# Kernel tuning notes

Hardware: AMD Instinct MI355X
Metric: run time of the kernel (lower is better)

## Reference

```python
import jax, jax.numpy as jnp
import numpy as np

B, T, D_IN, D_MODEL = 4, 4096, 256, 128


def setup_inputs() -> dict:
    key = jax.random.key(0)
    ks = jax.random.split(key, 7)
    s_in = 1.0 / np.sqrt(D_IN)
    return {
        "x": jax.random.normal(ks[0], (B, T, D_IN), dtype=jnp.float32),
        "Wq": jax.random.normal(ks[1], (D_IN, D_MODEL), dtype=jnp.float32) * s_in,
        "bq": jnp.zeros((D_MODEL,), dtype=jnp.float32),
        "Wk": jax.random.normal(ks[2], (D_IN, D_MODEL), dtype=jnp.float32) * s_in,
        "bk": jnp.zeros((D_MODEL,), dtype=jnp.float32),
        "Wv": jax.random.normal(ks[3], (D_IN, D_MODEL), dtype=jnp.float32) * s_in,
        "bv": jnp.zeros((D_MODEL,), dtype=jnp.float32),
    }


def reference(x, Wq, bq, Wk, bk, Wv, bv):
    # projections: (B,T,d_in) @ (d_in,d_model) -> (B,T,d_model)
    q = x @ Wq + bq
    k = x @ Wk + bk
    v = x @ Wv + bv
    # scores: (B,T,T), scaled by sqrt(d_model)
    scores = jnp.einsum("btd,bsd->bts", q, k) / np.sqrt(D_MODEL).astype(np.float32)
    attn = jax.nn.softmax(scores, axis=-1)
    out = jnp.einsum("bts,bsd->btd", attn, v)
    return out, attn
```

## Files before the change

### kernel.cpp

```cpp
#include <hip/hip_runtime.h>
#include <hip/hip_bf16.h>
#include <stdint.h>

#define TT 4096
#define DM 128
#define DIN 256
#define NB 4

typedef __attribute__((ext_vector_type(4))) float f32x4;
typedef __attribute__((ext_vector_type(8))) short s16x8;
typedef __attribute__((ext_vector_type(4))) short s16x4;

__device__ __forceinline__ unsigned short f2bf(float f) {
    union { float f; unsigned int u; } v; v.f = f;
    return (unsigned short)((v.u + 0x7FFFu + ((v.u >> 16) & 1u)) >> 16);
}
__device__ __forceinline__ float bf2f(unsigned short h) {
    union { unsigned int u; float f; } v; v.u = ((unsigned int)h) << 16;
    return v.f;
}

__device__ __forceinline__ void cp16(const void* g, void* l) {
    __builtin_amdgcn_global_load_lds(
        (__attribute__((address_space(1))) unsigned int*)(size_t)g,
        (__attribute__((address_space(3))) unsigned int*)l, 16, 0, 0);
}

__global__ __launch_bounds__(256) void k_wt(const float* __restrict__ Wq,
                                            const float* __restrict__ Wk,
                                            const float* __restrict__ Wv,
                                            unsigned short* __restrict__ Wtb) {
    int tid = blockIdx.x * 256 + threadIdx.x;
    int m = tid >> 15;
    int r = tid & 32767;
    int n = r >> 8;
    int k = r & 255;
    const float* W = (m == 0) ? Wq : (m == 1) ? Wk : Wv;
    Wtb[(size_t)tid] = f2bf(W[k * DM + n]);
}

__global__ __launch_bounds__(256) void k_proj(const float* __restrict__ x,
        const float* __restrict__ bq, const float* __restrict__ bk, const float* __restrict__ bv,
        const unsigned short* __restrict__ Wtb,
        unsigned short* __restrict__ Qb, unsigned short* __restrict__ Kb,
        unsigned short* __restrict__ Vb) {
    __shared__ __align__(16) unsigned short wt[DM][40];
    __shared__ __align__(16) unsigned short xl[64][40];
    int m = blockIdx.x >> 8;
    int tile = blockIdx.x & 255;
    int rowbase = tile * 64;
    int i = threadIdx.x;
    int w = i >> 6, l = i & 63;
    int lg = l >> 4, ll = l & 15;
    const float* bias = (m == 0) ? bq : (m == 1) ? bk : bv;
    unsigned short* out = (m == 0) ? Qb : (m == 1) ? Kb : Vb;
    const unsigned short* wsrc = Wtb + (size_t)m * DM * DIN;

    f32x4 acc[8];
    for (int n = 0; n < 8; n++) acc[n] = (f32x4){0.f, 0.f, 0.f, 0.f};

    for (int kk = 0; kk < 8; kk++) {
        int k0 = kk * 32;
        for (int t = 0; t < 2; t++) {
            int idx = i + t * 256;
            int row = idx >> 2, c8 = idx & 3;
            s16x8 v = *(const s16x8*)(wsrc + (size_t)row * DIN + k0 + c8 * 8);
            *(s16x8*)(&wt[row][c8 * 8]) = v;
        }
        for (int t = 0; t < 2; t++) {
            int idx = i + t * 256;
            int row = idx >> 3, c4 = idx & 7;
            f32x4 v = *(const f32x4*)(x + (size_t)(rowbase + row) * DIN + k0 + c4 * 4);
            s16x4 h;
            for (int j = 0; j < 4; j++) h[j] = (short)f2bf(v[j]);
            *(s16x4*)(&xl[row][c4 * 4]) = h;
        }
        __syncthreads();
        s16x8 a = *(const s16x8*)(&xl[w * 16 + ll][lg * 8]);
        for (int n = 0; n < 8; n++) {
            s16x8 b = *(const s16x8*)(&wt[n * 16 + ll][lg * 8]);
            acc[n] = __builtin_amdgcn_mfma_f32_16x16x32_bf16(a, b, acc[n], 0, 0, 0);
        }
        __syncthreads();
    }
    for (int n = 0; n < 8; n++) {
        int col = n * 16 + ll;
        float bv_ = bias[col];
        for (int j = 0; j < 4; j++) {
            int row = rowbase + w * 16 + lg * 4 + j;
            out[(size_t)row * DM + col] = f2bf(acc[n][j] + bv_);
        }
    }
}

__global__ __launch_bounds__(256) void k_vt(const unsigned short* __restrict__ Vb,
                                            unsigned short* __restrict__ Vtb) {
    __shared__ __align__(16) unsigned short tile[64][72];
    int bid = blockIdx.x;
    int b = bid >> 7;
    int rem = bid & 127;
    int tI = rem >> 1, dI = rem & 1;
    int t0 = tI * 64, d0 = dI * 64;
    int i = threadIdx.x;
    for (int t = 0; t < 2; t++) {
        int idx = i + t * 256;
        int r = idx >> 3, c8 = idx & 7;
        s16x8 v = *(const s16x8*)(Vb + ((size_t)(b * TT) + t0 + r) * DM + d0 + c8 * 8);
        *(s16x8*)(&tile[r][c8 * 8]) = v;
    }
    __syncthreads();
    for (int t = 0; t < 2; t++) {
        int idx = i + t * 256;
        int r2 = idx >> 3, c8 = idx & 7;
        s16x8 v;
        for (int j = 0; j < 8; j++) v[j] = (short)tile[c8 * 8 + j][r2];
        *(s16x8*)(Vtb + ((size_t)b * DM + d0 + r2) * TT + t0 + c8 * 8) = v;
    }
}

__global__ __launch_bounds__(256, 4) void k_rowsum(const unsigned short* __restrict__ Qb,
        const unsigned short* __restrict__ Kb, float* __restrict__ rsum8) {
    __shared__ __align__(16) char smem[24576];

    int bid = blockIdx.x;
    int id2 = (bid & 7) * 256 + (bid >> 3);
    int b = id2 >> 9;
    int rem = id2 & 511;
    int rt = rem >> 2, kq = rem & 3;
    int rowbase = rt * 32;
    int i = threadIdx.x;
    int w = i >> 6, l = i & 63;
    int rg = w & 1, ks = w >> 1;
    int lg = l >> 4, ll = l & 15;

    const unsigned short* Qrow = Qb + ((size_t)(b * TT) + rowbase) * DM;
    const unsigned short* Krow = Kb + (size_t)(b * TT) * DM + (size_t)(kq * 1024) * DM;
    const float scale = 0.08838834764831845f;

    s16x8 qf[4];
    for (int c = 0; c < 4; c++)
        qf[c] = *(const s16x8*)(Qrow + (size_t)(rg * 16 + ll) * DM + c * 32 + lg * 8);

    int kr = ks * 16 + ll;
    auto stage = [&](char* kbuf, int t) {
        int s0 = t * 32;
        for (int u = 0; u < 2; u++) {
            int c = u * 4 + w;
            int row = c * 4 + (l >> 4);
            int g = (l & 15) ^ (row & 7);
            cp16(Krow + (size_t)(s0 + row) * DM + g * 8, kbuf + c * 1024);
        }
    };

    float rs[4] = {0.f, 0.f, 0.f, 0.f};
    stage(smem, 0);
    stage(smem + 8192, 1);
    asm volatile("s_waitcnt vmcnt(2)" ::: "memory");
    __builtin_amdgcn_s_barrier();

    int cur = 0, nxt = 2;
    for (int t = 0; t < 32; t++) {
        int tn = (t + 2 <= 31) ? t + 2 : 31;
        stage(smem + nxt * 8192, tn);
        const char* kbase = smem + cur * 8192 + kr * 256;
        f32x4 a0 = (f32x4){0.f, 0.f, 0.f, 0.f}, a1 = (f32x4){0.f, 0.f, 0.f, 0.f};
        {
            s16x8 k0 = *(const s16x8*)(kbase + (((0 * 4 + lg) ^ (kr & 7)) << 4));
            s16x8 k1 = *(const s16x8*)(kbase + (((1 * 4 + lg) ^ (kr & 7)) << 4));
            s16x8 k2 = *(const s16x8*)(kbase + (((2 * 4 + lg) ^ (kr & 7)) << 4));
            s16x8 k3 = *(const s16x8*)(kbase + (((3 * 4 + lg) ^ (kr & 7)) << 4));
            a0 = __builtin_amdgcn_mfma_f32_16x16x32_bf16(qf[0], k0, a0, 0, 0, 0);
            a1 = __builtin_amdgcn_mfma_f32_16x16x32_bf16(qf[1], k1, a1, 0, 0, 0);
            a0 = __builtin_amdgcn_mfma_f32_16x16x32_bf16(qf[2], k2, a0, 0, 0, 0);
            a1 = __builtin_amdgcn_mfma_f32_16x16x32_bf16(qf[3], k3, a1, 0, 0, 0);
        }
        f32x4 acc;
        for (int j = 0; j < 4; j++) acc[j] = a0[j] + a1[j];
        for (int j = 0; j < 4; j++) rs[j] += __expf(acc[j] * scale);
        asm volatile("s_waitcnt vmcnt(2)" ::: "memory");
        __builtin_amdgcn_s_barrier();
        cur++; if (cur == 3) cur = 0;
        nxt++; if (nxt == 3) nxt = 0;
    }
    for (int mm = 1; mm < 16; mm <<= 1)
        for (int j = 0; j < 4; j++) rs[j] += __shfl_xor(rs[j], mm, 64);
    if (ll == 0) {
        int p = kq * 2 + ks;
        float* dst = rsum8 + ((size_t)(b * 8 + p)) * TT + rowbase + rg * 16 + lg * 4;
        for (int j = 0; j < 4; j++) dst[j] = rs[j];
    }
}


__global__ __launch_bounds__(256, 2) void k_attn(const unsigned short* __restrict__ Qb,
        const unsigned short* __restrict__ Kb, const unsigned short* __restrict__ Vtb,
        const float* __restrict__ rsum8,
        float* __restrict__ outO, float* __restrict__ outA) {
    __shared__ __align__(16) char smem[70656];

    int bid = blockIdx.x;
    int id2 = (bid & 7) * 64 + (bid >> 3);
    int b = id2 >> 7;
    int rowbase = (id2 & 127) * 32;
    int i = threadIdx.x;
    int w = i >> 6, l = i & 63;
    int rg = w & 1, ks = w >> 1;
    int lg = l >> 4, ll = l & 15;

    const unsigned short* Qrow = Qb + ((size_t)(b * TT) + rowbase) * DM;
    const unsigned short* Krow = Kb + (size_t)(b * TT) * DM;
    const unsigned short* Vt_b = Vtb + (size_t)b * DM * TT;
    const float scale = 0.08838834764831845f;

    unsigned short* Pw = (unsigned short*)(smem + 65536 + w * 1280);

    s16x8 qf[4];
    for (int c = 0; c < 4; c++)
        qf[c] = *(const s16x8*)(Qrow + (size_t)(rg * 16 + ll) * DM + c * 32 + lg * 8);

    float inv_[4];
    for (int j = 0; j < 4; j++) {
        int row = rowbase + rg * 16 + lg * 4 + j;
        float s = 0.f;
        for (int p = 0; p < 8; p++) s += rsum8[((size_t)(b * 8 + p)) * TT + row];
        inv_[j] = 1.0f / s;
    }

    int kr = ks * 16 + ll;
    auto stage = [&](char* slot, int t) {
        int s0 = t * 32;
        for (int u = 0; u < 2; u++) {
            int c = u * 4 + w;
            int row = c * 4 + (l >> 4);
            int g = (l & 15) ^ (row & 7);
            cp16(Krow + (size_t)(s0 + row) * DM + g * 8, slot + c * 1024);
        }
        for (int u = 0; u < 2; u++) {
            int c = u * 4 + w;
            int row = c * 16 + (l >> 2);
            int g = (l & 3) ^ (row & 3);
            cp16(Vt_b + (size_t)row * TT + s0 + g * 8, slot + 8192 + c * 1024);
        }
    };

    for (int j = 0; j < 4; j++) Pw[(lg * 4 + j) * 40 + 16 + ll] = 0;
    f32x4 oacc[8];
    for (int n = 0; n < 8; n++) oacc[n] = (f32x4){0.f, 0.f, 0.f, 0.f};

    stage(smem, 0);
    stage(smem + 16384, 1);
    stage(smem + 32768, 2);
    asm volatile("s_waitcnt vmcnt(8)" ::: "memory");
    __builtin_amdgcn_s_barrier();

    for (int t = 0; t < 128; t++) {
        int s0 = t * 32;
        int tn = (t + 3 <= 127) ? t + 3 : 127;
        stage(smem + ((t + 3) & 3) * 16384, tn);

        const char* kbase = smem + (t & 3) * 16384 + kr * 256;
        f32x4 a0 = (f32x4){0.f, 0.f, 0.f, 0.f}, a1 = (f32x4){0.f, 0.f, 0.f, 0.f};
        {
            s16x8 k0 = *(const s16x8*)(kbase + (((0 * 4 + lg) ^ (kr & 7)) << 4));
            s16x8 k1 = *(const s16x8*)(kbase + (((1 * 4 + lg) ^ (kr & 7)) << 4));
            s16x8 k2 = *(const s16x8*)(kbase + (((2 * 4 + lg) ^ (kr & 7)) << 4));
            s16x8 k3 = *(const s16x8*)(kbase + (((3 * 4 + lg) ^ (kr & 7)) << 4));
            a0 = __builtin_amdgcn_mfma_f32_16x16x32_bf16(qf[0], k0, a0, 0, 0, 0);
            a1 = __builtin_amdgcn_mfma_f32_16x16x32_bf16(qf[1], k1, a1, 0, 0, 0);
            a0 = __builtin_amdgcn_mfma_f32_16x16x32_bf16(qf[2], k2, a0, 0, 0, 0);
            a1 = __builtin_amdgcn_mfma_f32_16x16x32_bf16(qf[3], k3, a1, 0, 0, 0);
        }
        for (int j = 0; j < 4; j++) {
            float p = __expf((a0[j] + a1[j]) * scale) * inv_[j];
            Pw[(lg * 4 + j) * 40 + ll] = f2bf(p);
        }
        asm volatile("s_waitcnt lgkmcnt(0)" ::: "memory");
        __builtin_amdgcn_sched_barrier(0);
        {
            s16x8 paf = *(const s16x8*)(Pw + ll * 40 + lg * 8);
            const char* vbuf = smem + (t & 3) * 16384 + 8192;
            int gl = ks * 2 + (lg & 1);
            for (int n8 = 0; n8 < 8; n8++) {
                int row = n8 * 16 + ll;
                s16x8 bfr = *(const s16x8*)(vbuf + row * 64 + ((gl ^ (row & 3)) << 4));
                oacc[n8] = __builtin_amdgcn_mfma_f32_16x16x32_bf16(paf, bfr, oacc[n8], 0, 0, 0);
            }
        }
        {
            int arow = l >> 2, acol = (l & 3) * 4;
            s16x4 pv = *(const s16x4*)(Pw + arow * 40 + acol);
            f32x4 fv;
            for (int q = 0; q < 4; q++) fv[q] = bf2f((unsigned short)pv[q]);
            __builtin_nontemporal_store(fv,
                (f32x4*)(outA + ((size_t)(b * TT) + rowbase + rg * 16 + arow) * TT
                         + s0 + ks * 16 + acol));
        }
        asm volatile("s_waitcnt vmcnt(9)" ::: "memory");
        __builtin_amdgcn_s_barrier();
    }

    asm volatile("s_waitcnt vmcnt(0)" ::: "memory");
    __builtin_amdgcn_s_barrier();
    float* obuf = (float*)smem;
    if (ks == 1) {
        float* dst = obuf + (size_t)rg * 2112;
        for (int n8 = 0; n8 < 8; n8++)
            for (int j = 0; j < 4; j++)
                dst[(lg * 4 + j) * 132 + n8 * 16 + ll] = oacc[n8][j];
    }
    __syncthreads();
    if (ks == 0) {
        float* dst = obuf + (size_t)rg * 2112;
        for (int n8 = 0; n8 < 8; n8++)
            for (int j = 0; j < 4; j++) {
                int idx = (lg * 4 + j) * 132 + n8 * 16 + ll;
                dst[idx] += oacc[n8][j];
            }
    }
    __syncthreads();
    {
        int row = i >> 3;
        int colf = (i & 7) * 16;
        const float* src = obuf + (size_t)(row >> 4) * 2112 + (row & 15) * 132 + colf;
        float* dst = outO + ((size_t)(b * TT) + rowbase + row) * DM + colf;
        for (int u = 0; u < 4; u++)
            *(f32x4*)(dst + u * 4) = *(const f32x4*)(src + u * 4);
    }
}

extern "C" void kernel_launch(void* const* d_in, const int* in_sizes, int n_in,
                              void* d_out, int out_size, void* d_ws, size_t ws_size,
                              hipStream_t stream) {
    const float* x  = (const float*)d_in[0];
    const float* Wq = (const float*)d_in[1];
    const float* bq = (const float*)d_in[2];
    const float* Wk = (const float*)d_in[3];
    const float* bk = (const float*)d_in[4];
    const float* Wv = (const float*)d_in[5];
    const float* bv = (const float*)d_in[6];
    float* outO = (float*)d_out;
    float* outA = outO + (size_t)NB * TT * DM;

    char* ws = (char*)d_ws;
    unsigned short* Qb  = (unsigned short*)(ws);
    unsigned short* Kb  = (unsigned short*)(ws + ((size_t)1 << 22));
    unsigned short* Vb  = (unsigned short*)(ws + ((size_t)2 << 22));
    unsigned short* Vtb = (unsigned short*)(ws + ((size_t)3 << 22));
    unsigned short* Wtb = (unsigned short*)(ws + ((size_t)4 << 22));
    float* rsum8 = (float*)(ws + ((size_t)2 << 22));

    k_wt<<<dim3(384), dim3(256), 0, stream>>>(Wq, Wk, Wv, Wtb);
    k_proj<<<dim3(768), dim3(256), 0, stream>>>(x, bq, bk, bv, Wtb, Qb, Kb, Vb);
    k_vt<<<dim3(512), dim3(256), 0, stream>>>(Vb, Vtb);
    k_rowsum<<<dim3(2048), dim3(256), 0, stream>>>(Qb, Kb, rsum8);
    k_attn<<<dim3(512), dim3(256), 0, stream>>>(Qb, Kb, Vtb, rsum8, outO, outA);
}
```

Measured before the change: 157.2 us.

## Split attention kernel into producer score waves and consumer PV waves

Rewrites the attention kernel with 512 threads, split into two roles. Four waves stage K, compute QK^T scores and exponentials, and write bf16 probabilities into a 4-slot LDS ring. Four other waves stage V and, one step behind, run the P·V MFMAs and the streaming stores of the attention matrix. This specialisation is meant to overlap the exp/score phase with the PV and store phase and to drop the cross-wave reduction of output accumulators. It adds s_setprio hints and raises k_rowsum occupancy, at the cost of more LDS per block and tighter barrier coupling between the two groups.

```diff
diff --git a/kernel.cpp b/kernel.cpp
--- a/kernel.cpp
+++ b/kernel.cpp
@@ -10,6 +10,7 @@
 typedef __attribute__((ext_vector_type(4))) float f32x4;
 typedef __attribute__((ext_vector_type(8))) short s16x8;
 typedef __attribute__((ext_vector_type(4))) short s16x4;
+typedef __attribute__((ext_vector_type(2))) unsigned int u32x2;
 
 __device__ __forceinline__ unsigned short f2bf(float f) {
     union { float f; unsigned int u; } v; v.f = f;
@@ -118,7 +119,7 @@
     }
 }
 
-__global__ __launch_bounds__(256, 4) void k_rowsum(const unsigned short* __restrict__ Qb,
+__global__ __launch_bounds__(256, 6) void k_rowsum(const unsigned short* __restrict__ Qb,
         const unsigned short* __restrict__ Kb, float* __restrict__ rsum8) {
     __shared__ __align__(16) char smem[24576];
 
@@ -191,12 +192,11 @@
     }
 }
 
-
-__global__ __launch_bounds__(256, 2) void k_attn(const unsigned short* __restrict__ Qb,
+__global__ __launch_bounds__(512, 4) void k_attn2(const unsigned short* __restrict__ Qb,
         const unsigned short* __restrict__ Kb, const unsigned short* __restrict__ Vtb,
         const float* __restrict__ rsum8,
         float* __restrict__ outO, float* __restrict__ outA) {
-    __shared__ __align__(16) char smem[70656];
+    __shared__ __align__(16) char smem[75776];
 
     int bid = blockIdx.x;
     int id2 = (bid & 7) * 64 + (bid >> 3);
@@ -204,127 +204,125 @@
     int rowbase = (id2 & 127) * 32;
     int i = threadIdx.x;
     int w = i >> 6, l = i & 63;
-    int rg = w & 1, ks = w >> 1;
     int lg = l >> 4, ll = l & 15;
+    int rh = w & 1;
 
     const unsigned short* Qrow = Qb + ((size_t)(b * TT) + rowbase) * DM;
     const unsigned short* Krow = Kb + (size_t)(b * TT) * DM;
     const unsigned short* Vt_b = Vtb + (size_t)b * DM * TT;
     const float scale = 0.08838834764831845f;
 
-    unsigned short* Pw = (unsigned short*)(smem + 65536 + w * 1280);
-
-    s16x8 qf[4];
-    for (int c = 0; c < 4; c++)
-        qf[c] = *(const s16x8*)(Qrow + (size_t)(rg * 16 + ll) * DM + c * 32 + lg * 8);
-
-    float inv_[4];
-    for (int j = 0; j < 4; j++) {
-        int row = rowbase + rg * 16 + lg * 4 + j;
-        float s = 0.f;
-        for (int p = 0; p < 8; p++) s += rsum8[((size_t)(b * 8 + p)) * TT + row];
-        inv_[j] = 1.0f / s;
-    }
-
-    int kr = ks * 16 + ll;
-    auto stage = [&](char* slot, int t) {
+    char* kslotb = smem;
+    char* vslotb = smem + 32768;
+    unsigned short* PbB = (unsigned short*)(smem + 65536);
+
+    int kh = w >> 1;
+    int kr2 = kh * 16 + ll;
+    int cw = w - 4;
+    int r2 = cw & 1, c2 = cw >> 1;
+
+    auto stageK = [&](int slot, int t) {
         int s0 = t * 32;
         for (int u = 0; u < 2; u++) {
             int c = u * 4 + w;
             int row = c * 4 + (l >> 4);
             int g = (l & 15) ^ (row & 7);
-            cp16(Krow + (size_t)(s0 + row) * DM + g * 8, slot + c * 1024);
-        }
+            cp16(Krow + (size_t)(s0 + row) * DM + g * 8, kslotb + slot * 8192 + c * 1024);
+        }
+    };
+    auto stageV = [&](int slot, int t) {
+        int s0 = t * 32;
         for (int u = 0; u < 2; u++) {
-            int c = u * 4 + w;
+            int c = u * 4 + cw;
             int row = c * 16 + (l >> 2);
             int g = (l & 3) ^ (row & 3);
-            cp16(Vt_b + (size_t)row * TT + s0 + g * 8, slot + 8192 + c * 1024);
+            cp16(Vt_b + (size_t)row * TT + s0 + g * 8, vslotb + slot * 8192 + c * 1024);
         }
     };
 
-    for (int j = 0; j < 4; j++) Pw[(lg * 4 + j) * 40 + 16 + ll] = 0;
-    f32x4 oacc[8];
-    for (int n = 0; n < 8; n++) oacc[n] = (f32x4){0.f, 0.f, 0.f, 0.f};
-
-    stage(smem, 0);
-    stage(smem + 16384, 1);
-    stage(smem + 32768, 2);
-    asm volatile("s_waitcnt vmcnt(8)" ::: "memory");
-    __builtin_amdgcn_s_barrier();
-
-    for (int t = 0; t < 128; t++) {
-        int s0 = t * 32;
-        int tn = (t + 3 <= 127) ? t + 3 : 127;
-        stage(smem + ((t + 3) & 3) * 16384, tn);
-
-        const char* kbase = smem + (t & 3) * 16384 + kr * 256;
-        f32x4 a0 = (f32x4){0.f, 0.f, 0.f, 0.f}, a1 = (f32x4){0.f, 0.f, 0.f, 0.f};
+    if (w < 4) {
+        s16x8 qf[4];
+        for (int c = 0; c < 4; c++)
+            qf[c] = *(const s16x8*)(Qrow + (size_t)(rh * 16 + ll) * DM + c * 32 + lg * 8);
+        float inv;
         {
-            s16x8 k0 = *(const s16x8*)(kbase + (((0 * 4 + lg) ^ (kr & 7)) << 4));
-            s16x8 k1 = *(const s16x8*)(kbase + (((1 * 4 + lg) ^ (kr & 7)) << 4));
-            s16x8 k2 = *(const s16x8*)(kbase + (((2 * 4 + lg) ^ (kr & 7)) << 4));
-            s16x8 k3 = *(const s16x8*)(kbase + (((3 * 4 + lg) ^ (kr & 7)) << 4));
-            a0 = __builtin_amdgcn_mfma_f32_16x16x32_bf16(qf[0], k0, a0, 0, 0, 0);
-            a1 = __builtin_amdgcn_mfma_f32_16x16x32_bf16(qf[1], k1, a1, 0, 0, 0);
-            a0 = __builtin_amdgcn_mfma_f32_16x16x32_bf16(qf[2], k2, a0, 0, 0, 0);
-            a1 = __builtin_amdgcn_mfma_f32_16x16x32_bf16(qf[3], k3, a1, 0, 0, 0);
-        }
-        for (int j = 0; j < 4; j++) {
-            float p = __expf((a0[j] + a1[j]) * scale) * inv_[j];
-            Pw[(lg * 4 + j) * 40 + ll] = f2bf(p);
-        }
-        asm volatile("s_waitcnt lgkmcnt(0)" ::: "memory");
-        __builtin_amdgcn_sched_barrier(0);
-        {
-            s16x8 paf = *(const s16x8*)(Pw + ll * 40 + lg * 8);
-            const char* vbuf = smem + (t & 3) * 16384 + 8192;
-            int gl = ks * 2 + (lg & 1);
-            for (int n8 = 0; n8 < 8; n8++) {
-                int row = n8 * 16 + ll;
-                s16x8 bfr = *(const s16x8*)(vbuf + row * 64 + ((gl ^ (row & 3)) << 4));
-                oacc[n8] = __builtin_amdgcn_mfma_f32_16x16x32_bf16(paf, bfr, oacc[n8], 0, 0, 0);
+            int row = rowbase + rh * 16 + ll;
+            float s = 0.f;
+            for (int p = 0; p < 8; p++) s += rsum8[((size_t)(b * 8 + p)) * TT + row];
+            inv = 1.0f / s;
+        }
+        stageK(0, 0); stageK(1, 1);
+        asm volatile("s_waitcnt vmcnt(0)" ::: "memory");
+        __builtin_amdgcn_s_barrier();
+
+        for (int wd = 0; wd < 64; wd++) {
+            int t0 = 2 * wd;
+            if (wd < 63) { stageK((t0 + 2) & 3, t0 + 2); stageK((t0 + 3) & 3, t0 + 3); }
+            for (int s = 0; s < 2; s++) {
+                int t = t0 + s;
+                const char* kbase = kslotb + (t & 3) * 8192 + kr2 * 256;
+                f32x4 acc = (f32x4){0.f, 0.f, 0.f, 0.f};
+                __builtin_amdgcn_s_setprio(1);
+                for (int c = 0; c < 4; c++) {
+                    s16x8 kf = *(const s16x8*)(kbase + (((c * 4 + lg) ^ (kr2 & 7)) << 4));
+                    acc = __builtin_amdgcn_mfma_f32_16x16x32_bf16(kf, qf[c], acc, 0, 0, 0);
+                }
+                __builtin_amdgcn_s_setprio(0);
+                f32x4 p;
+                for (int j = 0; j < 4; j++) p[j] = __expf(acc[j] * scale) * inv;
+                int prow = rh * 16 + ll;
+                u32x2 pb;
+                pb[0] = (unsigned)f2bf(p[0]) | ((unsigned)f2bf(p[1]) << 16);
+                pb[1] = (unsigned)f2bf(p[2]) | ((unsigned)f2bf(p[3]) << 16);
+                *(u32x2*)(PbB + (t & 3) * 1280 + prow * 40 + kh * 16 + lg * 4) = pb;
             }
-        }
-        {
-            int arow = l >> 2, acol = (l & 3) * 4;
-            s16x4 pv = *(const s16x4*)(Pw + arow * 40 + acol);
+            asm volatile("s_waitcnt lgkmcnt(0)" ::: "memory");
+            asm volatile("s_waitcnt vmcnt(0)" ::: "memory");
+            __builtin_amdgcn_s_barrier();
+        }
+    } else {
+        f32x4 oacc[4];
+        for (int n = 0; n < 4; n++) oacc[n] = (f32x4){0.f, 0.f, 0.f, 0.f};
+
+        auto ctile = [&](int u) {
+            unsigned short* Pslot = PbB + (u & 3) * 1280;
+            s16x8 pa = *(const s16x8*)(Pslot + (r2 * 16 + ll) * 40 + lg * 8);
+            const char* vb = vslotb + (u & 3) * 8192;
+            __builtin_amdgcn_s_setprio(1);
+            for (int n8 = 0; n8 < 4; n8++) {
+                int vr = c2 * 64 + n8 * 16 + ll;
+                s16x8 bf = *(const s16x8*)(vb + vr * 64 + ((lg ^ (vr & 3)) << 4));
+                oacc[n8] = __builtin_amdgcn_mfma_f32_16x16x32_bf16(pa, bf, oacc[n8], 0, 0, 0);
+            }
+            __builtin_amdgcn_s_setprio(0);
+            int arow = cw * 8 + (l >> 3);
+            int acol = (l & 7) * 4;
+            s16x4 pv = *(const s16x4*)(Pslot + arow * 40 + acol);
             f32x4 fv;
             for (int q = 0; q < 4; q++) fv[q] = bf2f((unsigned short)pv[q]);
             __builtin_nontemporal_store(fv,
-                (f32x4*)(outA + ((size_t)(b * TT) + rowbase + rg * 16 + arow) * TT
-                         + s0 + ks * 16 + acol));
-        }
-        asm volatile("s_waitcnt vmcnt(9)" ::: "memory");
+                (f32x4*)(outA + ((size_t)(b * TT) + rowbase + arow) * TT
+                         + (size_t)u * 32 + acol));
+        };
+
+        for (int wd = 0; wd < 64; wd++) {
+            __builtin_amdgcn_s_barrier();
+            int t0 = 2 * wd;
+            stageV(t0 & 3, t0); stageV((t0 + 1) & 3, t0 + 1);
+            if (wd == 1)      asm volatile("s_waitcnt vmcnt(4)" ::: "memory");
+            else if (wd >= 2) asm volatile("s_waitcnt vmcnt(6)" ::: "memory");
+            if (wd >= 1) { ctile(t0 - 2); ctile(t0 - 1); }
+        }
         __builtin_amdgcn_s_barrier();
-    }
-
-    asm volatile("s_waitcnt vmcnt(0)" ::: "memory");
-    __builtin_amdgcn_s_barrier();
-    float* obuf = (float*)smem;
-    if (ks == 1) {
-        float* dst = obuf + (size_t)rg * 2112;
-        for (int n8 = 0; n8 < 8; n8++)
-            for (int j = 0; j < 4; j++)
-                dst[(lg * 4 + j) * 132 + n8 * 16 + ll] = oacc[n8][j];
-    }
-    __syncthreads();
-    if (ks == 0) {
-        float* dst = obuf + (size_t)rg * 2112;
-        for (int n8 = 0; n8 < 8; n8++)
+        asm volatile("s_waitcnt vmcnt(0)" ::: "memory");
+        ctile(126); ctile(127);
+
+        for (int n8 = 0; n8 < 4; n8++)
             for (int j = 0; j < 4; j++) {
-                int idx = (lg * 4 + j) * 132 + n8 * 16 + ll;
-                dst[idx] += oacc[n8][j];
+                int row = r2 * 16 + lg * 4 + j;
+                int col = c2 * 64 + n8 * 16 + ll;
+                outO[((size_t)(b * TT) + rowbase + row) * DM + col] = oacc[n8][j];
             }
-    }
-    __syncthreads();
-    {
-        int row = i >> 3;
-        int colf = (i & 7) * 16;
-        const float* src = obuf + (size_t)(row >> 4) * 2112 + (row & 15) * 132 + colf;
-        float* dst = outO + ((size_t)(b * TT) + rowbase + row) * DM + colf;
-        for (int u = 0; u < 4; u++)
-            *(f32x4*)(dst + u * 4) = *(const f32x4*)(src + u * 4);
     }
 }
 
@@ -347,11 +345,11 @@
     unsigned short* Vb  = (unsigned short*)(ws + ((size_t)2 << 22));
     unsigned short* Vtb = (unsigned short*)(ws + ((size_t)3 << 22));
     unsigned short* Wtb = (unsigned short*)(ws + ((size_t)4 << 22));
-    float* rsum8 = (float*)(ws + ((size_t)2 << 22));
+    float* rsum8 = (float*)(ws + ((size_t)5 << 22));
 
     k_wt<<<dim3(384), dim3(256), 0, stream>>>(Wq, Wk, Wv, Wtb);
     k_proj<<<dim3(768), dim3(256), 0, stream>>>(x, bq, bk, bv, Wtb, Qb, Kb, Vb);
     k_vt<<<dim3(512), dim3(256), 0, stream>>>(Vb, Vtb);
     k_rowsum<<<dim3(2048), dim3(256), 0, stream>>>(Qb, Kb, rsum8);
-    k_attn<<<dim3(512), dim3(256), 0, stream>>>(Qb, Kb, Vtb, rsum8, outO, outA);
-}
+    k_attn2<<<dim3(512), dim3(512), 0, stream>>>(Qb, Kb, Vtb, rsum8, outO, outA);
+}
```

New measurement: 133.7 us. 14.9% less time.
